# Kernel optimization log

Measured on AMD Instinct MI355X. Metric: run time of the kernel, lower is better.

The kernel has to match this reference:

```python
import jax, jax.numpy as jnp
import numpy as np

BATCH, NEURONS, N_FEAT, IN_DIM, OUT_DIM = 256, 1024, 1024, 256, 128


def setup_inputs() -> dict:
    key = jax.random.key(0)
    kx, kg, kv, kw = jax.random.split(key, 4)
    x = jax.random.normal(kx, (BATCH, N_FEAT, IN_DIM), dtype=jnp.float32)
    G = jax.random.normal(kg, (NEURONS, N_FEAT), dtype=jnp.float32)
    # Original initializes v, w to zeros; use randn so outputs/grads are non-trivial.
    v = jax.random.normal(kv, (NEURONS, IN_DIM, OUT_DIM), dtype=jnp.float32)
    w = jax.random.normal(kw, (NEURONS, IN_DIM, OUT_DIM), dtype=jnp.float32)
    return {"x": x, "G": G, "v": v, "w": w}


def reference(x, G, v, w):
    # Original math: out[i,m] = sum_{j,k,l} G[j,k] * x[i,k,l] * (v - w)[j,l,m]
    # Reordered contraction: first G @ x (sum over feature axis k),
    # avoiding the quadratic (batch, neurons, n, in_dim) intermediate.
    Gx = jnp.einsum('jk,ikl->ijl', G, x)          # (batch, neurons, in_dim)
    return jnp.einsum('ijl,jlm->im', Gx, v - w)    # (batch, out_dim)
```

## Files before the change

kernel.cpp:

```cpp
#include <hip/hip_runtime.h>
#include <hip/hip_bf16.h>


typedef __attribute__((ext_vector_type(8))) short bf16x8;
typedef __attribute__((ext_vector_type(4))) float f32x4;

#define AS1C(p) ((const __attribute__((address_space(1))) void*)(p))
#define AS3(p)  ((__attribute__((address_space(3))) void*)(p))

__device__ __forceinline__ unsigned short f2bf(float f) {
    unsigned u = __float_as_uint(f);
    unsigned r = u + 0x7fffu + ((u >> 16) & 1u);
    return (unsigned short)(r >> 16);
}

__global__ void prep_G(const float* __restrict__ G, unsigned short* __restrict__ Gt) {
    __shared__ float tile[32][33];
    int k0 = blockIdx.x * 32, j0 = blockIdx.y * 32;
    int tx = threadIdx.x, ty = threadIdx.y;
    #pragma unroll
    for (int r = 0; r < 32; r += 8)
        tile[ty + r][tx] = G[(size_t)(j0 + ty + r) * 1024 + k0 + tx];
    __syncthreads();
    #pragma unroll
    for (int r = 0; r < 32; r += 8)
        Gt[(size_t)(k0 + ty + r) * 1024 + j0 + tx] = f2bf(tile[tx][ty + r]);
}

__global__ void prep_D(const float* __restrict__ v, const float* __restrict__ w,
                       unsigned short* __restrict__ Dt) {
    __shared__ unsigned short tile[32][132];
    int j0 = blockIdx.x * 32;
    int l  = blockIdx.y;
    int t  = threadIdx.x;
    #pragma unroll
    for (int it = 0; it < 16; ++it) {
        int idx = it * 256 + t;
        int j = idx >> 7, m = idx & 127;
        size_t g = (size_t)(j0 + j) * 32768 + (size_t)l * 128 + m;
        tile[j][m] = f2bf(v[g] - w[g]);
    }
    __syncthreads();
    int m = t >> 1, half = t & 1;
    unsigned short vals[16];
    #pragma unroll
    for (int q = 0; q < 16; ++q) vals[q] = tile[half * 16 + q][m];
    size_t dst = ((size_t)m * 256 + l) * 1024 + j0 + half * 16;
    *(uint4*)(Dt + dst)     = *(uint4*)(vals);
    *(uint4*)(Dt + dst + 8) = *(uint4*)(vals + 8);
}

__global__ __launch_bounds__(256) void gemm1(const unsigned short* __restrict__ Gt,
                                             const unsigned short* __restrict__ Dt,
                                             unsigned short* __restrict__ Tt) {
    __shared__ __align__(16) unsigned short As[128 * 32];
    __shared__ __align__(16) unsigned short Bs[128 * 32];
    int tid = threadIdx.x, wv = tid >> 6, lane = tid & 63;
    int k0 = blockIdx.x * 128, n0 = blockIdx.y * 128;
    int ldrow = lane >> 2, ldcol = (lane & 3) * 8;
    int wr = (wv >> 1) * 64, wc = (wv & 1) * 64;
    int quad = lane >> 4, l15 = lane & 15;

    f32x4 acc[4][4] = {};

    for (int j0 = 0; j0 < 1024; j0 += 32) {
        #pragma unroll
        for (int i = 0; i < 2; ++i) {
            int r = wv * 32 + i * 16;
            __builtin_amdgcn_global_load_lds(
                AS1C(Gt + (size_t)(k0 + r + ldrow) * 1024 + j0 + ldcol),
                AS3(As + r * 32), 16, 0, 0);
            __builtin_amdgcn_global_load_lds(
                AS1C(Dt + (size_t)(n0 + r + ldrow) * 1024 + j0 + ldcol),
                AS3(Bs + r * 32), 16, 0, 0);
        }
        __syncthreads();
        bf16x8 a[4], b[4];
        #pragma unroll
        for (int rt = 0; rt < 4; ++rt)
            a[rt] = *(const bf16x8*)(As + (wr + rt * 16 + l15) * 32 + quad * 8);
        #pragma unroll
        for (int ct = 0; ct < 4; ++ct)
            b[ct] = *(const bf16x8*)(Bs + (wc + ct * 16 + l15) * 32 + quad * 8);
        #pragma unroll
        for (int rt = 0; rt < 4; ++rt)
            #pragma unroll
            for (int ct = 0; ct < 4; ++ct)
                acc[rt][ct] = __builtin_amdgcn_mfma_f32_16x16x32_bf16(a[rt], b[ct], acc[rt][ct], 0, 0, 0);
        __syncthreads();
    }
    #pragma unroll
    for (int rt = 0; rt < 4; ++rt)
        #pragma unroll
        for (int ct = 0; ct < 4; ++ct) {
            int col = wc + ct * 16 + l15;
            int np  = n0 + col;
            int mm  = np >> 8, ll = np & 255;
            #pragma unroll
            for (int r = 0; r < 4; ++r) {
                int k = k0 + wr + rt * 16 + quad * 4 + r;
                Tt[(size_t)mm * 262144 + (size_t)k * 256 + ll] = f2bf(acc[rt][ct][r]);
            }
        }
}

__global__ __launch_bounds__(256) void gemm2(const float* __restrict__ x,
                                             const unsigned short* __restrict__ Tt,
                                             float* __restrict__ out) {
    __shared__ __align__(16) unsigned short Xs[64 * 32];
    __shared__ __align__(16) unsigned short Ts[128 * 32];
    int tid = threadIdx.x, wv = tid >> 6, lane = tid & 63;
    int i0 = blockIdx.x * 64;
    size_t kl0 = (size_t)blockIdx.y * 2048;
    int ldrow = lane >> 2, ldcol = (lane & 3) * 8;
    int wr = (wv >> 1) * 32, wc = (wv & 1) * 64;
    int quad = lane >> 4, l15 = lane & 15;

    f32x4 acc[2][4] = {};

    for (int it = 0; it < 64; ++it) {
        size_t kk = kl0 + it * 32;
        #pragma unroll
        for (int i = 0; i < 2; ++i) {
            int r = wv * 32 + i * 16;
            __builtin_amdgcn_global_load_lds(
                AS1C(Tt + (size_t)(r + ldrow) * 262144 + kk + ldcol),
                AS3(Ts + r * 32), 16, 0, 0);
        }
        #pragma unroll
        for (int i = 0; i < 2; ++i) {
            int f = tid + i * 256;
            int r = f >> 3, c = (f & 7) * 4;
            float4 xv = *(const float4*)(x + (size_t)(i0 + r) * 262144 + kk + c);
            unsigned short h[4] = {f2bf(xv.x), f2bf(xv.y), f2bf(xv.z), f2bf(xv.w)};
            *(uint2*)(Xs + r * 32 + c) = *(uint2*)h;
        }
        __syncthreads();
        bf16x8 a[2], b[4];
        #pragma unroll
        for (int rt = 0; rt < 2; ++rt)
            a[rt] = *(const bf16x8*)(Xs + (wr + rt * 16 + l15) * 32 + quad * 8);
        #pragma unroll
        for (int ct = 0; ct < 4; ++ct)
            b[ct] = *(const bf16x8*)(Ts + (wc + ct * 16 + l15) * 32 + quad * 8);
        #pragma unroll
        for (int rt = 0; rt < 2; ++rt)
            #pragma unroll
            for (int ct = 0; ct < 4; ++ct)
                acc[rt][ct] = __builtin_amdgcn_mfma_f32_16x16x32_bf16(a[rt], b[ct], acc[rt][ct], 0, 0, 0);
        __syncthreads();
    }
    #pragma unroll
    for (int rt = 0; rt < 2; ++rt)
        #pragma unroll
        for (int ct = 0; ct < 4; ++ct)
            #pragma unroll
            for (int r = 0; r < 4; ++r) {
                int i  = i0 + wr + rt * 16 + quad * 4 + r;
                int mo = wc + ct * 16 + l15;
                atomicAdd(&out[(size_t)i * 128 + mo], acc[rt][ct][r]);
            }
}

extern "C" void kernel_launch(void* const* d_in, const int* in_sizes, int n_in,
                              void* d_out, int out_size, void* d_ws, size_t ws_size,
                              hipStream_t stream) {
    const float* x = (const float*)d_in[0];
    const float* G = (const float*)d_in[1];
    const float* v = (const float*)d_in[2];
    const float* w = (const float*)d_in[3];
    float* out = (float*)d_out;

    char* ws = (char*)d_ws;
    unsigned short* Dt = (unsigned short*)(ws);
    unsigned short* Tt = (unsigned short*)(ws + 67108864);
    unsigned short* Gt = (unsigned short*)(ws + 134217728);

    hipMemsetAsync(d_out, 0, (size_t)256 * 128 * sizeof(float), stream);
    prep_G<<<dim3(32, 32), dim3(32, 8), 0, stream>>>(G, Gt);
    prep_D<<<dim3(32, 256), 256, 0, stream>>>(v, w, Dt);
    gemm1<<<dim3(8, 256), 256, 0, stream>>>(Gt, Dt, Tt);
    gemm2<<<dim3(4, 128), 256, 0, stream>>>(x, Tt, out);
}
```

Measured before the change: 678.8 us.

## Vectorize prep_D loads, stage gemm1 epilogue through LDS, split gemm2 K further

prep_D now reads v and w with float4 loads over 64-row tiles and writes 64-byte runs, replacing scalar loads and 32-byte writes. gemm1's epilogue stages the bf16 results in an LDS tile so each thread writes contiguous 16-byte chunks of Tt instead of scattered 2-byte stores. gemm2 halves the K span per block and doubles the grid, adding a launch-bounds occupancy hint; this gives more parallelism at the cost of twice as many atomic adds into the output. The aim is to cut uncoalesced memory traffic and improve occupancy across the memory-bound stages.

```diff
diff --git a/kernel.cpp b/kernel.cpp
--- a/kernel.cpp
+++ b/kernel.cpp
@@ -29,25 +29,31 @@
 
 __global__ void prep_D(const float* __restrict__ v, const float* __restrict__ w,
                        unsigned short* __restrict__ Dt) {
-    __shared__ unsigned short tile[32][132];
-    int j0 = blockIdx.x * 32;
+    __shared__ unsigned short tile[64][132];
+    int j0 = blockIdx.x * 64;
     int l  = blockIdx.y;
     int t  = threadIdx.x;
     #pragma unroll
-    for (int it = 0; it < 16; ++it) {
-        int idx = it * 256 + t;
-        int j = idx >> 7, m = idx & 127;
-        size_t g = (size_t)(j0 + j) * 32768 + (size_t)l * 128 + m;
-        tile[j][m] = f2bf(v[g] - w[g]);
+    for (int it = 0; it < 8; ++it) {
+        int f = it * 256 + t;
+        int j = f >> 5;
+        int c4 = (f & 31) * 4;
+        size_t g = (size_t)(j0 + j) * 32768 + (size_t)l * 128 + c4;
+        float4 a = *(const float4*)(v + g);
+        float4 b = *(const float4*)(w + g);
+        unsigned short h[4] = { f2bf(a.x - b.x), f2bf(a.y - b.y),
+                                f2bf(a.z - b.z), f2bf(a.w - b.w) };
+        *(uint2*)(&tile[j][c4]) = *(uint2*)h;
     }
     __syncthreads();
     int m = t >> 1, half = t & 1;
-    unsigned short vals[16];
-    #pragma unroll
-    for (int q = 0; q < 16; ++q) vals[q] = tile[half * 16 + q][m];
-    size_t dst = ((size_t)m * 256 + l) * 1024 + j0 + half * 16;
-    *(uint4*)(Dt + dst)     = *(uint4*)(vals);
-    *(uint4*)(Dt + dst + 8) = *(uint4*)(vals + 8);
+    unsigned short vals[32];
+    #pragma unroll
+    for (int q = 0; q < 32; ++q) vals[q] = tile[half * 32 + q][m];
+    size_t dst = ((size_t)m * 256 + l) * 1024 + j0 + half * 32;
+    #pragma unroll
+    for (int p = 0; p < 4; ++p)
+        *(uint4*)(Dt + dst + p * 8) = *(uint4*)(vals + p * 8);
 }
 
 __global__ __launch_bounds__(256) void gemm1(const unsigned short* __restrict__ Gt,
@@ -55,6 +61,7 @@
                                              unsigned short* __restrict__ Tt) {
     __shared__ __align__(16) unsigned short As[128 * 32];
     __shared__ __align__(16) unsigned short Bs[128 * 32];
+    __shared__ __align__(16) unsigned short Ct[64][136];
     int tid = threadIdx.x, wv = tid >> 6, lane = tid & 63;
     int k0 = blockIdx.x * 128, n0 = blockIdx.y * 128;
     int ldrow = lane >> 2, ldcol = (lane & 3) * 8;
@@ -89,36 +96,48 @@
                 acc[rt][ct] = __builtin_amdgcn_mfma_f32_16x16x32_bf16(a[rt], b[ct], acc[rt][ct], 0, 0, 0);
         __syncthreads();
     }
-    #pragma unroll
-    for (int rt = 0; rt < 4; ++rt)
-        #pragma unroll
-        for (int ct = 0; ct < 4; ++ct) {
-            int col = wc + ct * 16 + l15;
-            int np  = n0 + col;
-            int mm  = np >> 8, ll = np & 255;
-            #pragma unroll
-            for (int r = 0; r < 4; ++r) {
-                int k = k0 + wr + rt * 16 + quad * 4 + r;
-                Tt[(size_t)mm * 262144 + (size_t)k * 256 + ll] = f2bf(acc[rt][ct][r]);
-            }
-        }
-}
-
-__global__ __launch_bounds__(256) void gemm2(const float* __restrict__ x,
-                                             const unsigned short* __restrict__ Tt,
-                                             float* __restrict__ out) {
+    int mQ = n0 >> 8, l0 = n0 & 255;
+    #pragma unroll
+    for (int h = 0; h < 2; ++h) {
+        if ((wv >> 1) == h) {
+            #pragma unroll
+            for (int rt = 0; rt < 4; ++rt)
+                #pragma unroll
+                for (int ct = 0; ct < 4; ++ct)
+                    #pragma unroll
+                    for (int r = 0; r < 4; ++r)
+                        Ct[rt * 16 + quad * 4 + r][wc + ct * 16 + l15] = f2bf(acc[rt][ct][r]);
+        }
+        __syncthreads();
+        int row = tid >> 2, qo = (tid & 3) * 32;
+        size_t dst = (size_t)mQ * 262144 + (size_t)(k0 + h * 64 + row) * 256 + l0 + qo;
+        uint4 d0 = *(uint4*)(&Ct[row][qo]);
+        uint4 d1 = *(uint4*)(&Ct[row][qo + 8]);
+        uint4 d2 = *(uint4*)(&Ct[row][qo + 16]);
+        uint4 d3 = *(uint4*)(&Ct[row][qo + 24]);
+        *(uint4*)(Tt + dst)      = d0;
+        *(uint4*)(Tt + dst + 8)  = d1;
+        *(uint4*)(Tt + dst + 16) = d2;
+        *(uint4*)(Tt + dst + 24) = d3;
+        __syncthreads();
+    }
+}
+
+__global__ __launch_bounds__(256, 4) void gemm2(const float* __restrict__ x,
+                                                const unsigned short* __restrict__ Tt,
+                                                float* __restrict__ out) {
     __shared__ __align__(16) unsigned short Xs[64 * 32];
     __shared__ __align__(16) unsigned short Ts[128 * 32];
     int tid = threadIdx.x, wv = tid >> 6, lane = tid & 63;
     int i0 = blockIdx.x * 64;
-    size_t kl0 = (size_t)blockIdx.y * 2048;
+    size_t kl0 = (size_t)blockIdx.y * 1024;
     int ldrow = lane >> 2, ldcol = (lane & 3) * 8;
     int wr = (wv >> 1) * 32, wc = (wv & 1) * 64;
     int quad = lane >> 4, l15 = lane & 15;
 
     f32x4 acc[2][4] = {};
 
-    for (int it = 0; it < 64; ++it) {
+    for (int it = 0; it < 32; ++it) {
         size_t kk = kl0 + it * 32;
         #pragma unroll
         for (int i = 0; i < 2; ++i) {
@@ -132,7 +151,7 @@
             int f = tid + i * 256;
             int r = f >> 3, c = (f & 7) * 4;
             float4 xv = *(const float4*)(x + (size_t)(i0 + r) * 262144 + kk + c);
-            unsigned short h[4] = {f2bf(xv.x), f2bf(xv.y), f2bf(xv.z), f2bf(xv.w)};
+            unsigned short h[4] = { f2bf(xv.x), f2bf(xv.y), f2bf(xv.z), f2bf(xv.w) };
             *(uint2*)(Xs + r * 32 + c) = *(uint2*)h;
         }
         __syncthreads();
@@ -178,7 +197,7 @@
 
     hipMemsetAsync(d_out, 0, (size_t)256 * 128 * sizeof(float), stream);
     prep_G<<<dim3(32, 32), dim3(32, 8), 0, stream>>>(G, Gt);
-    prep_D<<<dim3(32, 256), 256, 0, stream>>>(v, w, Dt);
+    prep_D<<<dim3(16, 256), 256, 0, stream>>>(v, w, Dt);
     gemm1<<<dim3(8, 256), 256, 0, stream>>>(Gt, Dt, Tt);
-    gemm2<<<dim3(4, 128), 256, 0, stream>>>(x, Tt, out);
-}
+    gemm2<<<dim3(4, 256), 256, 0, stream>>>(x, Tt, out);
+}
```

Result: slower. 701.4 us (+3.3%).
